# Kernel optimization log

Measured on AMD Instinct MI355X. Metric: run time of the kernel, lower is better.

Reference implementation:

```python
import jax, jax.numpy as jnp
import numpy as np

B, T, D, H = 4, 2048, 1024, 16
DEPTH = D // H
MASK_NEG = 1e10


def setup_inputs() -> dict:
    key = jax.random.key(0)
    k1, k2, k3 = jax.random.split(key, 3)
    x = jax.random.normal(k1, (B, T, D), dtype=jnp.float32)
    w_attn = jax.random.normal(k2, (D, 3 * D), dtype=jnp.float32) * 0.02
    b_attn = jnp.zeros((3 * D,), dtype=jnp.float32)
    w_proj = jax.random.normal(k3, (D, D), dtype=jnp.float32) * 0.02
    b_proj = jnp.zeros((D,), dtype=jnp.float32)
    return {"x": x, "w_attn": w_attn, "b_attn": b_attn,
            "w_proj": w_proj, "b_proj": b_proj}


def _split_heads(t):
    # (B, T, D) -> (B, H, T, depth)
    return t.reshape(B, T, H, DEPTH).transpose(0, 2, 1, 3)


def reference(x, w_attn, b_attn, w_proj, b_proj):
    # fused QKV projection (GPT-2 conv1d == dense)
    qkv = x @ w_attn + b_attn                      # (B, T, 3D)
    q, k, v = jnp.split(qkv, 3, axis=2)
    q, k, v = _split_heads(q), _split_heads(k), _split_heads(v)
    present = jnp.stack([k, v], axis=1)            # (B, 2, H, T, depth)

    # scaled scores with additive causal mask (as in source: w*b - 1e10*(1-b))
    scores = jnp.einsum('bhqd,bhkd->bhqk', q, k) / jnp.sqrt(
        jnp.asarray(DEPTH, dtype=x.dtype))
    i = jnp.arange(T)[:, None]
    j = jnp.arange(T)[None, :]
    b = (i >= j).astype(scores.dtype)              # (T, T) lower-tri incl diag
    scores = scores * b - MASK_NEG * (1.0 - b)
    attn = jax.nn.softmax(scores, axis=-1)         # (B, H, T, T)

    out = jnp.einsum('bhqk,bhkd->bhqd', attn, v)   # (B, H, T, depth)
    out = out.transpose(0, 2, 1, 3).reshape(B, T, D)
    out = out @ w_proj + b_proj                    # (B, T, D)
    return out, present
```

## Files before the change

### kernel.cpp

```cpp
#include <hip/hip_runtime.h>
#include <hip/hip_bf16.h>
#include <cstdint>
#include <cstddef>

typedef __bf16 y8 __attribute__((ext_vector_type(8)));
typedef float f4 __attribute__((ext_vector_type(4)));
typedef unsigned short u16t;

#define NB 4
#define TT 2048
#define DD 1024
#define HH 16

static constexpr size_t OUT0 = (size_t)NB * TT * DD;
#define QSCALE 0.180336880111120426f

__device__ __forceinline__ u16t bf16r(float f) {
    union { float f; unsigned u; } x; x.f = f;
    return (u16t)((x.u + 0x7FFFu + ((x.u >> 16) & 1u)) >> 16);
}

__device__ __forceinline__ unsigned cvtpk(float lo, float hi) {
    unsigned r;
    asm("v_cvt_pk_bf16_f32 %0, %1, %2" : "=v"(r) : "v"(lo), "v"(hi));
    return r;
}

#define GLDS16(g, s) __builtin_amdgcn_global_load_lds( \
    (__attribute__((address_space(1))) void*)(g),      \
    (__attribute__((address_space(3))) void*)(s), 16, 0, 0)

__global__ __launch_bounds__(256)
void cvt_f32_bf16(const float* __restrict__ in, u16t* __restrict__ outp, int n) {
    int i = (blockIdx.x * 256 + threadIdx.x) * 8;
    if (i >= n) return;
    float4 a = *(const float4*)(in + i);
    float4 b = *(const float4*)(in + i + 4);
    union { u16t h[8]; uint4 q; } u;
    u.h[0] = bf16r(a.x); u.h[1] = bf16r(a.y); u.h[2] = bf16r(a.z); u.h[3] = bf16r(a.w);
    u.h[4] = bf16r(b.x); u.h[5] = bf16r(b.y); u.h[6] = bf16r(b.z); u.h[7] = bf16r(b.w);
    *(uint4*)(outp + i) = u.q;
}

__global__ __launch_bounds__(256)
void transpose_w(const float* __restrict__ in, u16t* __restrict__ outp, int Kd, int Nd) {
    __shared__ float tile[32][33];
    const int n0 = blockIdx.x * 32, k0 = blockIdx.y * 32;
    const int tx = threadIdx.x & 31, ty = threadIdx.x >> 5;
    for (int yy = ty; yy < 32; yy += 8)
        tile[yy][tx] = in[(size_t)(k0 + yy) * Nd + n0 + tx];
    __syncthreads();
    for (int yy = ty; yy < 32; yy += 8)
        outp[(size_t)(n0 + yy) * Kd + k0 + tx] = bf16r(tile[tx][yy]);
}

template<int MODE>
__global__ __launch_bounds__(256, 2)
void gemm_bt(const u16t* __restrict__ A, const u16t* __restrict__ Bt,
             const float* __restrict__ bias, float* __restrict__ C,
             float* __restrict__ pres, u16t* __restrict__ qb,
             u16t* __restrict__ kb, u16t* __restrict__ vtb,
             int M, int N, int K)
{
    __shared__ u16t ldsA[2][128 * 64];
    __shared__ u16t ldsB[2][128 * 64];
    const int tid = threadIdx.x;
    const int w = tid >> 6, l = tid & 63;
    const int wr = w >> 1, wc = w & 1;
    const int lr = l & 15, lq = l >> 4;
    const int bm = blockIdx.x * 128;
    const int bn = blockIdx.y * 128;

    auto stage = [&](int k0, int pi) {
#pragma unroll
        for (int c = 0; c < 4; ++c) {
            const int L = ((w * 64 + l) << 4) + (c << 12);
            const int row = L >> 7;
            const int col = (((L >> 4) & 7) ^ (row & 7)) << 3;
            GLDS16(A + (size_t)(bm + row) * K + k0 + col,
                   (char*)ldsA[pi] + (w << 10) + (c << 12));
            GLDS16(Bt + (size_t)(bn + row) * K + k0 + col,
                   (char*)ldsB[pi] + (w << 10) + (c << 12));
        }
    };

    f4 acc[4][4] = {};

    stage(0, 0);
    __syncthreads();
    int cur = 0;
    const int nt = K >> 6;
    for (int t = 0; t < nt; ++t) {
        if (t + 1 < nt) stage((t + 1) << 6, cur ^ 1);
        const char* La = (const char*)ldsA[cur];
        const char* Lb = (const char*)ldsB[cur];
#pragma unroll
        for (int ks = 0; ks < 2; ++ks) {
            y8 af[4], bfv[4];
#pragma unroll
            for (int m = 0; m < 4; ++m) {
                const int row = wr * 64 + m * 16 + lr;
                const int slot = (lq + ks * 4) ^ (row & 7);
                af[m] = *(const y8*)(La + row * 128 + (slot << 4));
            }
#pragma unroll
            for (int n = 0; n < 4; ++n) {
                const int row = wc * 64 + n * 16 + lr;
                const int slot = (lq + ks * 4) ^ (row & 7);
                bfv[n] = *(const y8*)(Lb + row * 128 + (slot << 4));
            }
#pragma unroll
            for (int m = 0; m < 4; ++m)
#pragma unroll
                for (int n = 0; n < 4; ++n)
                    acc[m][n] = __builtin_amdgcn_mfma_f32_16x16x32_bf16(af[m], bfv[n], acc[m][n], 0, 0, 0);
        }
        __syncthreads();
        cur ^= 1;
    }

    if (MODE == 0) {
#pragma unroll
        for (int m = 0; m < 4; ++m) {
            const int rowb = bm + wr * 64 + m * 16 + 4 * lq;
#pragma unroll
            for (int n = 0; n < 4; ++n) {
                const int col = bn + wc * 64 + n * 16 + lr;
                const float bv = bias[col];
#pragma unroll
                for (int r = 0; r < 4; ++r)
                    C[(size_t)(rowb + r) * N + col] = acc[m][n][r] + bv;
            }
        }
    } else {
        const int part = bn >> 10;
#pragma unroll
        for (int m = 0; m < 4; ++m) {
            const int rowb = bm + wr * 64 + m * 16 + 4 * lq;
            const int b0 = rowb >> 11, t0 = rowb & 2047;
#pragma unroll
            for (int n = 0; n < 4; ++n) {
                const int colg = bn + wc * 64 + n * 16 + lr;
                const float bv = bias[colg];
                const int cl = colg & 1023;
                const int h = cl >> 6, d = cl & 63;
                float vals[4];
#pragma unroll
                for (int r = 0; r < 4; ++r) vals[r] = acc[m][n][r] + bv;
                if (part == 0) {
#pragma unroll
                    for (int r = 0; r < 4; ++r)
                        qb[(((size_t)(b0 * HH + h)) * TT + t0 + r) * 64 + d] =
                            bf16r(vals[r] * QSCALE);
                } else if (part == 1) {
#pragma unroll
                    for (int r = 0; r < 4; ++r) {
                        kb[(((size_t)(b0 * HH + h)) * TT + t0 + r) * 64 + d] = bf16r(vals[r]);
                        pres[OUT0 + (((size_t)((b0 * 2 + 0) * HH + h)) * TT + t0 + r) * 64 + d] = vals[r];
                    }
                } else {
#pragma unroll
                    for (int r = 0; r < 4; ++r)
                        pres[OUT0 + (((size_t)((b0 * 2 + 1) * HH + h)) * TT + t0 + r) * 64 + d] = vals[r];
                    uint2 pk;
                    pk.x = cvtpk(vals[0], vals[1]);
                    pk.y = cvtpk(vals[2], vals[3]);
                    *(uint2*)(vtb + ((size_t)(b0 * HH + h) * 64 + d) * TT + t0) = pk;
                }
            }
        }
    }
}

__global__ __launch_bounds__(256, 2)
void attn_fwd(const u16t* __restrict__ qg, const u16t* __restrict__ kg,
              const u16t* __restrict__ vtg, u16t* __restrict__ og)
{
    __shared__ u16t sQ[128 * 64];
    __shared__ u16t sK[2 * 64 * 64];
    __shared__ u16t sV[2 * 64 * 64];
    __shared__ u16t sP[4 * 32 * 64];
    const int tid = threadIdx.x;
    const int w = tid >> 6, l = tid & 63;
    const int lr = l & 15, lq = l >> 4;
    const int qt = 15 - blockIdx.y;
    const int bh = blockIdx.x;
    const int b = bh >> 4, h = bh & 15;
    const u16t* qsrc = qg + (size_t)bh * TT * 64;
    const u16t* ksrc = kg + (size_t)bh * TT * 64;
    const u16t* vsrc = vtg + (size_t)bh * 64 * TT;

    auto stageKV = [&](int kt, int pi) {
        const int kv0 = kt << 6;
#pragma unroll
        for (int c = 0; c < 2; ++c) {
            const int L = ((w * 64 + l) << 4) + (c << 12);
            const int row = L >> 7;
            const int col = (((L >> 4) & 7) ^ (row & 7)) << 3;
            GLDS16(ksrc + (kv0 + row) * 64 + col,
                   (char*)sK + (pi << 13) + (w << 10) + (c << 12));
            GLDS16(vsrc + (size_t)row * TT + kv0 + col,
                   (char*)sV + (pi << 13) + (w << 10) + (c << 12));
        }
    };

#pragma unroll
    for (int c = 0; c < 4; ++c) {
        const int L = ((w * 64 + l) << 4) + (c << 12);
        const int row = L >> 7;
        const int col = (((L >> 4) & 7) ^ (row & 7)) << 3;
        GLDS16(qsrc + (qt * 128 + row) * 64 + col, (char*)sQ + (w << 10) + (c << 12));
    }
    stageKV(0, 0);
    __syncthreads();

    y8 qf[2][2];
#pragma unroll
    for (int qm = 0; qm < 2; ++qm)
#pragma unroll
        for (int ks = 0; ks < 2; ++ks) {
            const int row = w * 32 + qm * 16 + lr;
            const int slot = (lq + ks * 4) ^ (row & 7);
            qf[qm][ks] = *(const y8*)((const char*)sQ + row * 128 + (slot << 4));
        }

    f4 o[2][4] = {};
    float mrow[2] = {-1e30f, -1e30f};
    float lsum[2] = {0.f, 0.f};

    char* Pw = (char*)sP + (w << 12);
    const int qmax = qt * 128 + w * 32 + 31;
    const int ktiles = 2 * qt + 2;
    int cur = 0;

    for (int kt = 0; kt < ktiles; ++kt) {
        __syncthreads();
        if (kt + 1 < ktiles) stageKV(kt + 1, cur ^ 1);
        const int kv0 = kt << 6;
        if (kv0 <= qmax) {
            const char* Kb = (const char*)sK + (cur << 13);
            const char* Vb = (const char*)sV + (cur << 13);

            f4 s[2][4] = {};
            __builtin_amdgcn_s_setprio(1);
#pragma unroll
            for (int ks = 0; ks < 2; ++ks) {
                y8 kf[4];
#pragma unroll
                for (int n = 0; n < 4; ++n) {
                    const int row = n * 16 + lr;
                    const int slot = (lq + ks * 4) ^ (row & 7);
                    kf[n] = *(const y8*)(Kb + row * 128 + (slot << 4));
                }
#pragma unroll
                for (int qm = 0; qm < 2; ++qm)
#pragma unroll
                    for (int n = 0; n < 4; ++n)
                        s[qm][n] = __builtin_amdgcn_mfma_f32_16x16x32_bf16(kf[n], qf[qm][ks], s[qm][n], 0, 0, 0);
            }
            __builtin_amdgcn_s_setprio(0);

#pragma unroll
            for (int qm = 0; qm < 2; ++qm) {
                const int qb0 = qt * 128 + w * 32 + qm * 16;
                if (kv0 + 63 > qb0) {
                    const int query = qb0 + lr;
#pragma unroll
                    for (int n = 0; n < 4; ++n)
#pragma unroll
                        for (int r = 0; r < 4; ++r)
                            if (kv0 + n * 16 + 4 * lq + r > query) s[qm][n][r] = -1e30f;
                }

                float mx = -1e30f;
#pragma unroll
                for (int n = 0; n < 4; ++n)
                    mx = fmaxf(mx, fmaxf(fmaxf(s[qm][n][0], s[qm][n][1]),
                                         fmaxf(s[qm][n][2], s[qm][n][3])));
                mx = fmaxf(mx, __shfl_xor(mx, 16));
                mx = fmaxf(mx, __shfl_xor(mx, 32));

                if (!__all(mx <= mrow[qm] + 8.f)) {
                    const float newm = fmaxf(mrow[qm], mx);
                    const float corr = exp2f(mrow[qm] - newm);
                    mrow[qm] = newm;
                    lsum[qm] *= corr;
#pragma unroll
                    for (int n = 0; n < 4; ++n) o[qm][n] *= corr;
                }

                float rs = 0.f;
#pragma unroll
                for (int n = 0; n < 4; ++n)
#pragma unroll
                    for (int r = 0; r < 4; ++r) {
                        const float p = exp2f(s[qm][n][r] - mrow[qm]);
                        s[qm][n][r] = p;
                        rs += p;
                    }
                lsum[qm] += rs;

                const int prow = qm * 16 + lr;
                const int rbase = prow * 128 + ((lq & 1) << 3);
#pragma unroll
                for (int n = 0; n < 4; ++n) {
                    uint2 pk;
                    pk.x = cvtpk(s[qm][n][0], s[qm][n][1]);
                    pk.y = cvtpk(s[qm][n][2], s[qm][n][3]);
                    const int sIdx = 2 * n + (lq >> 1);
                    *(uint2*)(Pw + rbase + ((sIdx ^ (prow & 7)) << 4)) = pk;
                }
            }

            __builtin_amdgcn_s_setprio(1);
#pragma unroll
            for (int ks = 0; ks < 2; ++ks) {
                y8 vf[4], pf[2];
#pragma unroll
                for (int n = 0; n < 4; ++n) {
                    const int row = n * 16 + lr;
                    const int slot = (lq + ks * 4) ^ (row & 7);
                    vf[n] = *(const y8*)(Vb + row * 128 + (slot << 4));
                }
#pragma unroll
                for (int qm = 0; qm < 2; ++qm) {
                    const int row = qm * 16 + lr;
                    const int slot = (lq + ks * 4) ^ (row & 7);
                    pf[qm] = *(const y8*)(Pw + row * 128 + (slot << 4));
                }
#pragma unroll
                for (int qm = 0; qm < 2; ++qm)
#pragma unroll
                    for (int n = 0; n < 4; ++n)
                        o[qm][n] = __builtin_amdgcn_mfma_f32_16x16x32_bf16(vf[n], pf[qm], o[qm][n], 0, 0, 0);
            }
            __builtin_amdgcn_s_setprio(0);
        }
        cur ^= 1;
    }

#pragma unroll
    for (int qm = 0; qm < 2; ++qm) {
        float t = lsum[qm];
        t += __shfl_xor(t, 16);
        t += __shfl_xor(t, 32);
        const float inv = 1.0f / t;
        const int trow = qt * 128 + w * 32 + qm * 16 + lr;
#pragma unroll
        for (int n = 0; n < 4; ++n) {
            uint2 pk;
            pk.x = cvtpk(o[qm][n][0] * inv, o[qm][n][1] * inv);
            pk.y = cvtpk(o[qm][n][2] * inv, o[qm][n][3] * inv);
            *(uint2*)(og + ((size_t)(b * TT + trow)) * DD + h * 64 + n * 16 + 4 * lq) = pk;
        }
    }
}

extern "C" void kernel_launch(void* const* d_in, const int* in_sizes, int n_in,
                              void* d_out, int out_size, void* d_ws, size_t ws_size,
                              hipStream_t stream) {
    const float* x      = (const float*)d_in[0];
    const float* w_attn = (const float*)d_in[1];
    const float* b_attn = (const float*)d_in[2];
    const float* w_proj = (const float*)d_in[3];
    const float* b_proj = (const float*)d_in[4];
    float* outp = (float*)d_out;
    char* ws = (char*)d_ws;

    u16t* xb  = (u16t*)(ws + 0);
    u16t* wta = (u16t*)(ws + 16777216);
    u16t* wtp = (u16t*)(ws + 23068672);
    u16t* qb  = (u16t*)(ws + 25165824);
    u16t* kb  = (u16t*)(ws + 41943040);
    u16t* vtb = (u16t*)(ws + 58720256);
    if (ws_size < 75497472) return;

    cvt_f32_bf16<<<4096, 256, 0, stream>>>(x, xb, 8388608);
    transpose_w<<<dim3(96, 32), 256, 0, stream>>>(w_attn, wta, 1024, 3072);
    transpose_w<<<dim3(32, 32), 256, 0, stream>>>(w_proj, wtp, 1024, 1024);

    gemm_bt<1><<<dim3(64, 24), 256, 0, stream>>>(xb, wta, b_attn, nullptr, outp,
                                                 qb, kb, vtb, 8192, 3072, 1024);
    attn_fwd<<<dim3(64, 16), 256, 0, stream>>>(qb, kb, vtb, xb );
    gemm_bt<0><<<dim3(64, 8), 256, 0, stream>>>(xb, wtp, b_proj, outp,
                                                nullptr, nullptr, nullptr, nullptr,
                                                8192, 1024, 1024);
}
```

Measured before the change: 195.5 us.

## Replace QKV GEMM with 256x256-tile 8-wave phased pipelined kernel

```diff
diff --git a/kernel.cpp b/kernel.cpp
--- a/kernel.cpp
+++ b/kernel.cpp
@@ -29,6 +29,10 @@
 #define GLDS16(g, s) __builtin_amdgcn_global_load_lds( \
     (__attribute__((address_space(1))) void*)(g),      \
     (__attribute__((address_space(3))) void*)(s), 16, 0, 0)
+
+#define BARX() asm volatile("s_barrier" ::: "memory")
+#define VMW(n) asm volatile("s_waitcnt vmcnt(" #n ")" ::: "memory")
+#define LGKM0() asm volatile("s_waitcnt lgkmcnt(0)" ::: "memory")
 
 __global__ __launch_bounds__(256)
 void cvt_f32_bf16(const float* __restrict__ in, u16t* __restrict__ outp, int n) {
@@ -54,13 +58,151 @@
         outp[(size_t)(n0 + yy) * Kd + k0 + tx] = bf16r(tile[tx][yy]);
 }
 
-template<int MODE>
+__global__ __launch_bounds__(512, 1)
+void qkv_gemm_8ph(const u16t* __restrict__ A, const u16t* __restrict__ Bt,
+                  const float* __restrict__ bias, float* __restrict__ pres,
+                  u16t* __restrict__ qb, u16t* __restrict__ kb, u16t* __restrict__ vtb)
+{
+    constexpr int K = DD;
+    constexpr int NT = K / 64;
+    __shared__ u16t ldsA[2][256 * 64];
+    __shared__ u16t ldsB[2][256 * 64];
+    const int tid = threadIdx.x;
+    const int w = tid >> 6, l = tid & 63;
+    const int wm = w >> 2, wn = w & 3;
+    const int lr = l & 15, lq = l >> 4;
+    const int bm = blockIdx.x * 256;
+    const int bn = blockIdx.y * 256;
+
+    auto stageA = [&](int t, int h) {
+        if (t >= NT) return;
+        const int d = t & 1;
+#pragma unroll
+        for (int c = 0; c < 2; ++c) {
+            const int L = tid * 16 + (c << 13);
+            const int row = L >> 7;
+            const int col = (((L >> 4) & 7) ^ (row & 7)) << 3;
+            GLDS16(A + (size_t)(bm + h * 128 + row) * K + t * 64 + col,
+                   (char*)ldsA[d] + (h << 14) + (c << 13) + (w << 10));
+        }
+    };
+    auto stageB = [&](int t, int h) {
+        if (t >= NT) return;
+        const int d = t & 1;
+#pragma unroll
+        for (int c = 0; c < 2; ++c) {
+            const int L = tid * 16 + (c << 13);
+            const int row = L >> 7;
+            const int col = (((L >> 4) & 7) ^ (row & 7)) << 3;
+            GLDS16(Bt + (size_t)(bn + h * 128 + row) * K + t * 64 + col,
+                   (char*)ldsB[d] + (h << 14) + (c << 13) + (w << 10));
+        }
+    };
+
+    y8 af[4][2];
+    y8 bf[2][2][2];
+    f4 acc[8][4] = {};
+
+    auto ldAf = [&](int d, int qm) {
+#pragma unroll
+        for (int ks = 0; ks < 2; ++ks)
+#pragma unroll
+            for (int m = 0; m < 4; ++m) {
+                const int row = wm * 128 + qm * 64 + m * 16 + lr;
+                const int slot = (lq + ks * 4) ^ (row & 7);
+                af[m][ks] = *(const y8*)((const char*)ldsA[d] + row * 128 + (slot << 4));
+            }
+    };
+    auto ldBf = [&](int d, int qn) {
+#pragma unroll
+        for (int ks = 0; ks < 2; ++ks)
+#pragma unroll
+            for (int n = 0; n < 2; ++n) {
+                const int row = wn * 64 + qn * 32 + n * 16 + lr;
+                const int slot = (lq + ks * 4) ^ (row & 7);
+                bf[qn][n][ks] = *(const y8*)((const char*)ldsB[d] + row * 128 + (slot << 4));
+            }
+    };
+    auto mfmaQ = [&](int qm, int qn) {
+        __builtin_amdgcn_s_setprio(1);
+#pragma unroll
+        for (int ks = 0; ks < 2; ++ks)
+#pragma unroll
+            for (int m = 0; m < 4; ++m)
+#pragma unroll
+                for (int n = 0; n < 2; ++n)
+                    acc[qm * 4 + m][qn * 2 + n] = __builtin_amdgcn_mfma_f32_16x16x32_bf16(
+                        af[m][ks], bf[qn][n][ks], acc[qm * 4 + m][qn * 2 + n], 0, 0, 0);
+        __builtin_amdgcn_s_setprio(0);
+    };
+
+    stageA(0, 0); stageA(0, 1); stageB(0, 0); stageB(0, 1);
+    stageB(1, 0); stageB(1, 1);
+    VMW(4);
+    BARX();
+
+    for (int it = 0; it < NT / 2; ++it) {
+        const int t0 = 2 * it;
+        const bool last = (it == NT / 2 - 1);
+#pragma unroll
+        for (int g = 0; g < 2; ++g) {
+            ldAf(g, 0); ldBf(g, 0);
+            stageA(t0 + 1 + g, 0);
+            BARX(); LGKM0(); mfmaQ(0, 0); BARX();
+            ldBf(g, 1);
+            stageA(t0 + 1 + g, 1);
+            BARX(); LGKM0(); mfmaQ(0, 1); BARX();
+            ldAf(g, 1);
+            stageB(t0 + 2 + g, 0);
+            BARX(); LGKM0(); mfmaQ(1, 0); BARX();
+            stageB(t0 + 2 + g, 1);
+            if (last) { VMW(0); } else { VMW(4); }
+            BARX(); mfmaQ(1, 1); BARX();
+        }
+    }
+
+    const int part = bn >> 10;
+#pragma unroll
+    for (int mf = 0; mf < 8; ++mf) {
+        const int rowb = bm + wm * 128 + mf * 16 + 4 * lq;
+        const int b0 = rowb >> 11, tr0 = rowb & 2047;
+#pragma unroll
+        for (int nf = 0; nf < 4; ++nf) {
+            const int colg = bn + wn * 64 + nf * 16 + lr;
+            const float bv = bias[colg];
+            const int cl = colg & 1023;
+            const int h = cl >> 6, d = cl & 63;
+            float vals[4];
+#pragma unroll
+            for (int r = 0; r < 4; ++r) vals[r] = acc[mf][nf][r] + bv;
+            if (part == 0) {
+#pragma unroll
+                for (int r = 0; r < 4; ++r)
+                    qb[(((size_t)(b0 * HH + h)) * TT + tr0 + r) * 64 + d] =
+                        bf16r(vals[r] * QSCALE);
+            } else if (part == 1) {
+#pragma unroll
+                for (int r = 0; r < 4; ++r) {
+                    kb[(((size_t)(b0 * HH + h)) * TT + tr0 + r) * 64 + d] = bf16r(vals[r]);
+                    pres[OUT0 + (((size_t)((b0 * 2 + 0) * HH + h)) * TT + tr0 + r) * 64 + d] = vals[r];
+                }
+            } else {
+#pragma unroll
+                for (int r = 0; r < 4; ++r)
+                    pres[OUT0 + (((size_t)((b0 * 2 + 1) * HH + h)) * TT + tr0 + r) * 64 + d] = vals[r];
+                uint2 pk;
+                pk.x = cvtpk(vals[0], vals[1]);
+                pk.y = cvtpk(vals[2], vals[3]);
+                *(uint2*)(vtb + ((size_t)(b0 * HH + h) * 64 + d) * TT + tr0) = pk;
+            }
+        }
+    }
+}
+
 __global__ __launch_bounds__(256, 2)
-void gemm_bt(const u16t* __restrict__ A, const u16t* __restrict__ Bt,
-             const float* __restrict__ bias, float* __restrict__ C,
-             float* __restrict__ pres, u16t* __restrict__ qb,
-             u16t* __restrict__ kb, u16t* __restrict__ vtb,
-             int M, int N, int K)
+void gemm_proj(const u16t* __restrict__ A, const u16t* __restrict__ Bt,
+               const float* __restrict__ bias, float* __restrict__ C,
+               int M, int N, int K)
 {
     __shared__ u16t ldsA[2][128 * 64];
     __shared__ u16t ldsB[2][128 * 64];
@@ -119,55 +261,16 @@
         cur ^= 1;
     }
 
-    if (MODE == 0) {
-#pragma unroll
-        for (int m = 0; m < 4; ++m) {
-            const int rowb = bm + wr * 64 + m * 16 + 4 * lq;
-#pragma unroll
-            for (int n = 0; n < 4; ++n) {
-                const int col = bn + wc * 64 + n * 16 + lr;
-                const float bv = bias[col];
-#pragma unroll
-                for (int r = 0; r < 4; ++r)
-                    C[(size_t)(rowb + r) * N + col] = acc[m][n][r] + bv;
-            }
-        }
-    } else {
-        const int part = bn >> 10;
-#pragma unroll
-        for (int m = 0; m < 4; ++m) {
-            const int rowb = bm + wr * 64 + m * 16 + 4 * lq;
-            const int b0 = rowb >> 11, t0 = rowb & 2047;
-#pragma unroll
-            for (int n = 0; n < 4; ++n) {
-                const int colg = bn + wc * 64 + n * 16 + lr;
-                const float bv = bias[colg];
-                const int cl = colg & 1023;
-                const int h = cl >> 6, d = cl & 63;
-                float vals[4];
-#pragma unroll
-                for (int r = 0; r < 4; ++r) vals[r] = acc[m][n][r] + bv;
-                if (part == 0) {
-#pragma unroll
-                    for (int r = 0; r < 4; ++r)
-                        qb[(((size_t)(b0 * HH + h)) * TT + t0 + r) * 64 + d] =
-                            bf16r(vals[r] * QSCALE);
-                } else if (part == 1) {
-#pragma unroll
-                    for (int r = 0; r < 4; ++r) {
-                        kb[(((size_t)(b0 * HH + h)) * TT + t0 + r) * 64 + d] = bf16r(vals[r]);
-                        pres[OUT0 + (((size_t)((b0 * 2 + 0) * HH + h)) * TT + t0 + r) * 64 + d] = vals[r];
-                    }
-                } else {
-#pragma unroll
-                    for (int r = 0; r < 4; ++r)
-                        pres[OUT0 + (((size_t)((b0 * 2 + 1) * HH + h)) * TT + t0 + r) * 64 + d] = vals[r];
-                    uint2 pk;
-                    pk.x = cvtpk(vals[0], vals[1]);
-                    pk.y = cvtpk(vals[2], vals[3]);
-                    *(uint2*)(vtb + ((size_t)(b0 * HH + h) * 64 + d) * TT + t0) = pk;
-                }
-            }
+#pragma unroll
+    for (int m = 0; m < 4; ++m) {
+        const int rowb = bm + wr * 64 + m * 16 + 4 * lq;
+#pragma unroll
+        for (int n = 0; n < 4; ++n) {
+            const int col = bn + wc * 64 + n * 16 + lr;
+            const float bv = bias[col];
+#pragma unroll
+            for (int r = 0; r < 4; ++r)
+                C[(size_t)(rowb + r) * N + col] = acc[m][n][r] + bv;
         }
     }
 }
@@ -379,10 +482,7 @@
     transpose_w<<<dim3(96, 32), 256, 0, stream>>>(w_attn, wta, 1024, 3072);
     transpose_w<<<dim3(32, 32), 256, 0, stream>>>(w_proj, wtp, 1024, 1024);
 
-    gemm_bt<1><<<dim3(64, 24), 256, 0, stream>>>(xb, wta, b_attn, nullptr, outp,
-                                                 qb, kb, vtb, 8192, 3072, 1024);
+    qkv_gemm_8ph<<<dim3(32, 12), 512, 0, stream>>>(xb, wta, b_attn, outp, qb, kb, vtb);
     attn_fwd<<<dim3(64, 16), 256, 0, stream>>>(qb, kb, vtb, xb );
-    gemm_bt<0><<<dim3(64, 8), 256, 0, stream>>>(xb, wtp, b_proj, outp,
-                                                nullptr, nullptr, nullptr, nullptr,
-                                                8192, 1024, 1024);
-}
+    gemm_proj<<<dim3(64, 8), 256, 0, stream>>>(xb, wtp, b_proj, outp, 8192, 1024, 1024);
+}
```

Result: no change. 195.7 us (+0.1%).

## Make GEMM persistent over multiple tiles with cross-tile prefetch and manual waitcnt

Applied to the files above, without the earlier changes.

```diff
diff --git a/kernel.cpp b/kernel.cpp
--- a/kernel.cpp
+++ b/kernel.cpp
@@ -29,6 +29,9 @@
 #define GLDS16(g, s) __builtin_amdgcn_global_load_lds( \
     (__attribute__((address_space(1))) void*)(g),      \
     (__attribute__((address_space(3))) void*)(s), 16, 0, 0)
+
+#define BARX() asm volatile("s_barrier" ::: "memory")
+#define VMW(n) asm volatile("s_waitcnt vmcnt(" #n ")" ::: "memory")
 
 __global__ __launch_bounds__(256)
 void cvt_f32_bf16(const float* __restrict__ in, u16t* __restrict__ outp, int n) {
@@ -54,13 +57,13 @@
         outp[(size_t)(n0 + yy) * Kd + k0 + tx] = bf16r(tile[tx][yy]);
 }
 
-template<int MODE>
+template<int MODE, int TPB>
 __global__ __launch_bounds__(256, 2)
 void gemm_bt(const u16t* __restrict__ A, const u16t* __restrict__ Bt,
              const float* __restrict__ bias, float* __restrict__ C,
              float* __restrict__ pres, u16t* __restrict__ qb,
              u16t* __restrict__ kb, u16t* __restrict__ vtb,
-             int M, int N, int K)
+             int N, int K)
 {
     __shared__ u16t ldsA[2][128 * 64];
     __shared__ u16t ldsB[2][128 * 64];
@@ -68,10 +71,8 @@
     const int w = tid >> 6, l = tid & 63;
     const int wr = w >> 1, wc = w & 1;
     const int lr = l & 15, lq = l >> 4;
-    const int bm = blockIdx.x * 128;
-    const int bn = blockIdx.y * 128;
-
-    auto stage = [&](int k0, int pi) {
+
+    auto stage = [&](int bm, int bn, int k0, int pi) {
 #pragma unroll
         for (int c = 0; c < 4; ++c) {
             const int L = ((w * 64 + l) << 4) + (c << 12);
@@ -84,88 +85,100 @@
         }
     };
 
-    f4 acc[4][4] = {};
-
-    stage(0, 0);
-    __syncthreads();
-    int cur = 0;
     const int nt = K >> 6;
-    for (int t = 0; t < nt; ++t) {
-        if (t + 1 < nt) stage((t + 1) << 6, cur ^ 1);
-        const char* La = (const char*)ldsA[cur];
-        const char* Lb = (const char*)ldsB[cur];
-#pragma unroll
-        for (int ks = 0; ks < 2; ++ks) {
-            y8 af[4], bfv[4];
+
+#pragma unroll
+    for (int j = 0; j < TPB; ++j) {
+        const int idx = blockIdx.x * TPB + j;
+        const int bm = (idx & 63) << 7;
+        const int bn = (idx >> 6) << 7;
+
+        f4 acc[4][4] = {};
+        if (j == 0) stage(bm, bn, 0, 0);
+
+        for (int t = 0; t < nt; ++t) {
+            if (t + 1 < nt) {
+                stage(bm, bn, (t + 1) << 6, (t + 1) & 1);
+            } else if (j + 1 < TPB) {
+                const int nx = idx + 1;
+                stage((nx & 63) << 7, (nx >> 6) << 7, 0, 0);
+            }
+            if (t + 1 == nt && j + 1 == TPB) { VMW(0); } else { VMW(8); }
+            BARX();
+            const char* La = (const char*)ldsA[t & 1];
+            const char* Lb = (const char*)ldsB[t & 1];
+#pragma unroll
+            for (int ks = 0; ks < 2; ++ks) {
+                y8 af[4], bfv[4];
+#pragma unroll
+                for (int m = 0; m < 4; ++m) {
+                    const int row = wr * 64 + m * 16 + lr;
+                    const int slot = (lq + ks * 4) ^ (row & 7);
+                    af[m] = *(const y8*)(La + row * 128 + (slot << 4));
+                }
+#pragma unroll
+                for (int n = 0; n < 4; ++n) {
+                    const int row = wc * 64 + n * 16 + lr;
+                    const int slot = (lq + ks * 4) ^ (row & 7);
+                    bfv[n] = *(const y8*)(Lb + row * 128 + (slot << 4));
+                }
+#pragma unroll
+                for (int m = 0; m < 4; ++m)
+#pragma unroll
+                    for (int n = 0; n < 4; ++n)
+                        acc[m][n] = __builtin_amdgcn_mfma_f32_16x16x32_bf16(af[m], bfv[n], acc[m][n], 0, 0, 0);
+            }
+            BARX();
+        }
+
+        if (MODE == 0) {
 #pragma unroll
             for (int m = 0; m < 4; ++m) {
-                const int row = wr * 64 + m * 16 + lr;
-                const int slot = (lq + ks * 4) ^ (row & 7);
-                af[m] = *(const y8*)(La + row * 128 + (slot << 4));
-            }
-#pragma unroll
-            for (int n = 0; n < 4; ++n) {
-                const int row = wc * 64 + n * 16 + lr;
-                const int slot = (lq + ks * 4) ^ (row & 7);
-                bfv[n] = *(const y8*)(Lb + row * 128 + (slot << 4));
-            }
-#pragma unroll
-            for (int m = 0; m < 4; ++m)
-#pragma unroll
-                for (int n = 0; n < 4; ++n)
-                    acc[m][n] = __builtin_amdgcn_mfma_f32_16x16x32_bf16(af[m], bfv[n], acc[m][n], 0, 0, 0);
-        }
-        __syncthreads();
-        cur ^= 1;
-    }
-
-    if (MODE == 0) {
-#pragma unroll
-        for (int m = 0; m < 4; ++m) {
-            const int rowb = bm + wr * 64 + m * 16 + 4 * lq;
-#pragma unroll
-            for (int n = 0; n < 4; ++n) {
-                const int col = bn + wc * 64 + n * 16 + lr;
-                const float bv = bias[col];
-#pragma unroll
-                for (int r = 0; r < 4; ++r)
-                    C[(size_t)(rowb + r) * N + col] = acc[m][n][r] + bv;
-            }
-        }
-    } else {
-        const int part = bn >> 10;
-#pragma unroll
-        for (int m = 0; m < 4; ++m) {
-            const int rowb = bm + wr * 64 + m * 16 + 4 * lq;
-            const int b0 = rowb >> 11, t0 = rowb & 2047;
-#pragma unroll
-            for (int n = 0; n < 4; ++n) {
-                const int colg = bn + wc * 64 + n * 16 + lr;
-                const float bv = bias[colg];
-                const int cl = colg & 1023;
-                const int h = cl >> 6, d = cl & 63;
-                float vals[4];
-#pragma unroll
-                for (int r = 0; r < 4; ++r) vals[r] = acc[m][n][r] + bv;
-                if (part == 0) {
+                const int rowb = bm + wr * 64 + m * 16 + 4 * lq;
+#pragma unroll
+                for (int n = 0; n < 4; ++n) {
+                    const int col = bn + wc * 64 + n * 16 + lr;
+                    const float bv = bias[col];
 #pragma unroll
                     for (int r = 0; r < 4; ++r)
-                        qb[(((size_t)(b0 * HH + h)) * TT + t0 + r) * 64 + d] =
-                            bf16r(vals[r] * QSCALE);
-                } else if (part == 1) {
-#pragma unroll
-                    for (int r = 0; r < 4; ++r) {
-                        kb[(((size_t)(b0 * HH + h)) * TT + t0 + r) * 64 + d] = bf16r(vals[r]);
-                        pres[OUT0 + (((size_t)((b0 * 2 + 0) * HH + h)) * TT + t0 + r) * 64 + d] = vals[r];
+                        C[(size_t)(rowb + r) * N + col] = acc[m][n][r] + bv;
+                }
+            }
+        } else {
+            const int part = bn >> 10;
+#pragma unroll
+            for (int m = 0; m < 4; ++m) {
+                const int rowb = bm + wr * 64 + m * 16 + 4 * lq;
+                const int b0 = rowb >> 11, t0 = rowb & 2047;
+#pragma unroll
+                for (int n = 0; n < 4; ++n) {
+                    const int colg = bn + wc * 64 + n * 16 + lr;
+                    const float bv = bias[colg];
+                    const int cl = colg & 1023;
+                    const int h = cl >> 6, d = cl & 63;
+                    float vals[4];
+#pragma unroll
+                    for (int r = 0; r < 4; ++r) vals[r] = acc[m][n][r] + bv;
+                    if (part == 0) {
+#pragma unroll
+                        for (int r = 0; r < 4; ++r)
+                            qb[(((size_t)(b0 * HH + h)) * TT + t0 + r) * 64 + d] =
+                                bf16r(vals[r] * QSCALE);
+                    } else if (part == 1) {
+#pragma unroll
+                        for (int r = 0; r < 4; ++r) {
+                            kb[(((size_t)(b0 * HH + h)) * TT + t0 + r) * 64 + d] = bf16r(vals[r]);
+                            pres[OUT0 + (((size_t)((b0 * 2 + 0) * HH + h)) * TT + t0 + r) * 64 + d] = vals[r];
+                        }
+                    } else {
+#pragma unroll
+                        for (int r = 0; r < 4; ++r)
+                            pres[OUT0 + (((size_t)((b0 * 2 + 1) * HH + h)) * TT + t0 + r) * 64 + d] = vals[r];
+                        uint2 pk;
+                        pk.x = cvtpk(vals[0], vals[1]);
+                        pk.y = cvtpk(vals[2], vals[3]);
+                        *(uint2*)(vtb + ((size_t)(b0 * HH + h) * 64 + d) * TT + t0) = pk;
                     }
-                } else {
-#pragma unroll
-                    for (int r = 0; r < 4; ++r)
-                        pres[OUT0 + (((size_t)((b0 * 2 + 1) * HH + h)) * TT + t0 + r) * 64 + d] = vals[r];
-                    uint2 pk;
-                    pk.x = cvtpk(vals[0], vals[1]);
-                    pk.y = cvtpk(vals[2], vals[3]);
-                    *(uint2*)(vtb + ((size_t)(b0 * HH + h) * 64 + d) * TT + t0) = pk;
                 }
             }
         }
@@ -379,10 +392,10 @@
     transpose_w<<<dim3(96, 32), 256, 0, stream>>>(w_attn, wta, 1024, 3072);
     transpose_w<<<dim3(32, 32), 256, 0, stream>>>(w_proj, wtp, 1024, 1024);
 
-    gemm_bt<1><<<dim3(64, 24), 256, 0, stream>>>(xb, wta, b_attn, nullptr, outp,
-                                                 qb, kb, vtb, 8192, 3072, 1024);
+    gemm_bt<1, 3><<<512, 256, 0, stream>>>(xb, wta, b_attn, nullptr, outp,
+                                           qb, kb, vtb, 3072, 1024);
     attn_fwd<<<dim3(64, 16), 256, 0, stream>>>(qb, kb, vtb, xb );
-    gemm_bt<0><<<dim3(64, 8), 256, 0, stream>>>(xb, wtp, b_proj, outp,
-                                                nullptr, nullptr, nullptr, nullptr,
-                                                8192, 1024, 1024);
-}
+    gemm_bt<0, 1><<<512, 256, 0, stream>>>(xb, wtp, b_proj, outp,
+                                           nullptr, nullptr, nullptr, nullptr,
+                                           1024, 1024);
+}
```

After: 194.0 us. No clear change (-0.7%).
